# Kernel optimization log

Measured on AMD Instinct MI355X. Metric: run time of the kernel, lower is better.

Reference implementation:

```python
import jax, jax.numpy as jnp
import numpy as np

N_NODES = 50000
N_EDGES = 800000
IN_CH = 8
CH = 128
EATTR = 6
N_BBOX = 2000
N_CLASSES = 32
N_BLOCKS = 3  # head + 2 residual blocks; n_blocks_out = 3
FUSION = CH * N_BLOCKS  # 384


def _kaiming(key, shape):
    fan_in = shape[0]
    return jax.random.normal(key, shape, dtype=jnp.float32) * np.sqrt(2.0 / fan_in)


def setup_inputs() -> dict:
    key = jax.random.key(0)
    ks = jax.random.split(key, 24)
    x = jax.random.normal(ks[0], (N_NODES, IN_CH), dtype=jnp.float32)
    e_attr = jax.random.normal(ks[1], (N_EDGES, EATTR), dtype=jnp.float32)
    edge = jax.random.randint(ks[2], (2, N_EDGES), 0, N_NODES, dtype=jnp.int32)
    bbox_idx = jnp.sort(jax.random.randint(ks[3], (N_NODES,), 0, N_BBOX, dtype=jnp.int32))
    d_head = 2 * IN_CH + EATTR   # 22
    d_blk = 2 * CH + EATTR       # 262
    inp = {
        "x": x, "e_attr": e_attr,
        "W_h": _kaiming(ks[4], (d_head, CH)), "b_h": jnp.zeros((CH,), jnp.float32),
        "Ws_h": _kaiming(ks[5], (d_head, CH)), "bs_h": jnp.zeros((CH,), jnp.float32),
        "Wb": jnp.stack([_kaiming(ks[6], (d_blk, CH)), _kaiming(ks[7], (d_blk, CH))]),
        "bb": jnp.zeros((2, CH), jnp.float32),
        "Wbs": jnp.stack([_kaiming(ks[8], (d_blk, CH)), _kaiming(ks[9], (d_blk, CH))]),
        "bbs": jnp.zeros((2, CH), jnp.float32),
        "W_f": _kaiming(ks[10], (FUSION, 1024)), "b_f": jnp.zeros((1024,), jnp.float32),
        "W_fs": _kaiming(ks[11], (FUSION, 1024)), "b_fs": jnp.zeros((1024,), jnp.float32),
        "W1": _kaiming(ks[12], ((FUSION + 1024) * 2, 512)), "b1": jnp.zeros((512,), jnp.float32),
        "W2": _kaiming(ks[13], (512, 256)), "b2": jnp.zeros((256,), jnp.float32),
        "W3": _kaiming(ks[14], (256, N_CLASSES)), "b3": jnp.zeros((N_CLASSES,), jnp.float32),
        "edge": edge, "bbox_idx": bbox_idx,
    }
    return inp


def _seg_max0(h, idx, n):
    m = jax.ops.segment_max(h, idx, num_segments=n)
    return jnp.where(jnp.isneginf(m), 0.0, m)  # empty segments -> 0 (torch_scatter semantics)


def _seg_mean(h, idx, n):
    s = jax.ops.segment_sum(h, idx, num_segments=n)
    c = jax.ops.segment_sum(jnp.ones((h.shape[0], 1), h.dtype), idx, num_segments=n)
    return s / jnp.maximum(c, 1.0)


def _graph_conv(x, x_node, src, dst, e_attr, W, b, Ws, bs, n):
    # edge message: MLP(concat(x_i, x_j - x_i, e_attr)); max-scatter for node stream,
    # mean-scatter for super stream (gp2 = two global-pool reductions)
    h = jax.nn.relu(jnp.concatenate([x[src], x[dst] - x[src], e_attr], axis=1) @ W + b)
    f = _seg_max0(h, dst, n)
    hs = jax.nn.relu(jnp.concatenate([x_node[src], x_node[dst] - x_node[src], e_attr], axis=1) @ Ws + bs)
    f_super = _seg_mean(hs, dst, n)
    return f, f_super


def reference(x, e_attr, W_h, b_h, Ws_h, bs_h, Wb, bb, Wbs, bbs,
              W_f, b_f, W_fs, b_fs, W1, b1, W2, b2, W3, b3, edge, bbox_idx):
    src, dst = edge[0], edge[1]
    n = x.shape[0]
    # head conv
    f, fs = _graph_conv(x, x, src, dst, e_attr, W_h, b_h, Ws_h, bs_h, n)
    feats, feats_super = [f], [fs]
    # residual blocks
    for i in range(N_BLOCKS - 1):
        g, gs = _graph_conv(feats[-1], feats_super[-1], src, dst, e_attr,
                            Wb[i], bb[i], Wbs[i], bbs[i], n)
        feats.append(g + feats[-1])
        feats_super.append(gs + feats_super[-1])
    feats = jnp.concatenate(feats, axis=1)              # [N, 384]
    fusion = jax.nn.relu(feats @ W_f + b_f)             # [N, 1024]
    out_feat = jnp.concatenate([fusion, feats], axis=1) # [N, 1408]
    feats_super = jnp.concatenate(feats_super, axis=1)  # [N, 384]
    feats_super = _seg_mean(feats_super, bbox_idx, N_BBOX)            # [B, 384]
    fusion_super = jax.nn.relu(feats_super @ W_fs + b_fs)             # [B, 1024]
    out_super = jnp.concatenate([fusion_super, feats_super], axis=1)  # [B, 1408]
    pooled = _seg_max0(out_feat, bbox_idx, N_BBOX)                    # [B, 1408]
    h = jnp.concatenate([pooled, out_super], axis=1)                  # [B, 2816]
    h = jax.nn.relu(h @ W1 + b1)
    h = jax.nn.relu(h @ W2 + b2)  # dropout=0 / eval mode
    logits = h @ W3 + b3          # classifier == 'softmax': raw logits returned
    return logits
```

## Files before the change

### kernel.cpp

```cpp
#include <hip/hip_runtime.h>
#include <stdint.h>

#define NN      50000
#define NN_PAD  50176
#define NE      800000
#define INCH    8
#define CH      128
#define EA      6
#define NB      2000
#define NB_PAD  2048
#define NCLS    32
#define FUS     384
#define K1      2816
#define SCAN_NBLK 49

typedef _Float16 half8 __attribute__((ext_vector_type(8)));
typedef _Float16 h2 __attribute__((ext_vector_type(2)));
typedef float f32x4 __attribute__((ext_vector_type(4)));

__global__ __launch_bounds__(256) void k_deg(const int* __restrict__ edge,
                                             int* __restrict__ deg) {
  int e = blockIdx.x * 256 + threadIdx.x;
  if (e < NE) atomicAdd(&deg[edge[NE + e]], 1);
}

__global__ __launch_bounds__(1024) void k_scan1(const int* __restrict__ deg,
                                                int* __restrict__ row_ptr,
                                                int* __restrict__ bsum) {
  __shared__ int wsum[16];
  const int t = threadIdx.x, lane = t & 63, w = t >> 6;
  const int i = blockIdx.x * 1024 + t;
  int x = (i < NN) ? deg[i] : 0;
#pragma unroll
  for (int off = 1; off < 64; off <<= 1) {
    int y = __shfl_up(x, off, 64);
    if (lane >= off) x += y;
  }
  if (lane == 63) wsum[w] = x;
  __syncthreads();
  if (w == 0 && lane < 16) {
    int s = wsum[lane];
#pragma unroll
    for (int off = 1; off < 16; off <<= 1) {
      int y = __shfl_up(s, off, 64);
      if (lane >= off) s += y;
    }
    wsum[lane] = s;
  }
  __syncthreads();
  int incl = x + ((w == 0) ? 0 : wsum[w - 1]);
  if (i < NN) row_ptr[i + 1] = incl;
  if (t == 1023) bsum[blockIdx.x] = incl;
}

__global__ __launch_bounds__(64) void k_scan2(int* __restrict__ bsum) {
  const int t = threadIdx.x;
  int x = (t < SCAN_NBLK) ? bsum[t] : 0;
#pragma unroll
  for (int off = 1; off < 64; off <<= 1) {
    int y = __shfl_up(x, off, 64);
    if (t >= off) x += y;
  }
  int ex = __shfl_up(x, 1, 64);
  if (t == 0) ex = 0;
  if (t < SCAN_NBLK) bsum[t] = ex;
}

__global__ __launch_bounds__(256) void k_scan3(const int* __restrict__ bsum,
                                               int* __restrict__ row_ptr) {
  const int i = blockIdx.x * 256 + threadIdx.x;
  if (i == 0) row_ptr[0] = 0;
  if (i < NN) row_ptr[i + 1] += bsum[i >> 10];
}

__global__ __launch_bounds__(256) void k_fill(
    const int* __restrict__ edge, const float* __restrict__ eattr,
    const int* __restrict__ row_ptr, int* __restrict__ cursor,
    int* __restrict__ ssrc, _Float16* __restrict__ sea8) {
  int e = blockIdx.x * 256 + threadIdx.x;
  if (e >= NE) return;
  int s = edge[e], d = edge[NE + e];
  int idx = row_ptr[d] + atomicAdd(&cursor[d], 1);
  ssrc[idx] = s;
  half8 v;
#pragma unroll
  for (int j = 0; j < EA; ++j) v[j] = (_Float16)eattr[(size_t)e * EA + j];
  v[6] = (_Float16)0.f; v[7] = (_Float16)0.f;
  *(half8*)(sea8 + (size_t)idx * 8) = v;
}

__global__ __launch_bounds__(256) void k_segstart(const int* __restrict__ bbox,
                                                  int* __restrict__ seg) {
  int i = blockIdx.x * 256 + threadIdx.x;
  if (i >= NN) return;
  int bc = bbox[i];
  int bp = (i == 0) ? -1 : bbox[i - 1];
  for (int j = bp + 1; j <= bc; ++j) seg[j] = i;
  if (i == NN - 1)
    for (int j = bc + 1; j <= NB; ++j) seg[j] = NN;
}

__global__ __launch_bounds__(256) void k_node_pq(
    const float* __restrict__ X, int ldx, int K,
    const float* __restrict__ WN, const float* __restrict__ bN,
    const float* __restrict__ WS, const float* __restrict__ bS,
    _Float16* __restrict__ PQi, _Float16* __restrict__ Qi) {
  const int sel = blockIdx.y;
  const float* W = sel ? WS : WN;
  const float* bias = sel ? bS : bN;
  const int t = threadIdx.x, lane = t & 63, wv = t >> 6;
  const int nbase = blockIdx.x * 32 + wv * 8;
  const int c = lane * 2;
  const float2 bv = *(const float2*)(bias + c);
  float2 pacc[8], qacc[8];
#pragma unroll
  for (int u = 0; u < 8; ++u) { pacc[u] = bv; qacc[u] = make_float2(0.f, 0.f); }
  const int xrow = min(nbase + (lane >> 3), NN - 1);
  const int xk = lane & 7;
  for (int k0 = 0; k0 < K; k0 += 8) {
    const float xv = X[(size_t)xrow * ldx + k0 + xk];
#pragma unroll
    for (int j = 0; j < 8; ++j) {
      const float2 w1 = *(const float2*)(W + (size_t)(k0 + j) * CH + c);
      const float2 w2 = *(const float2*)(W + (size_t)(K + k0 + j) * CH + c);
      const float2 wd = {w1.x - w2.x, w1.y - w2.y};
#pragma unroll
      for (int u = 0; u < 8; ++u) {
        const float xs = __shfl(xv, u * 8 + j, 64);
        pacc[u].x += xs * wd.x; pacc[u].y += xs * wd.y;
        qacc[u].x += xs * w2.x; qacc[u].y += xs * w2.y;
      }
    }
  }
#pragma unroll
  for (int u = 0; u < 8; ++u) {
    const int node = nbase + u;
    if (node < NN) {
      const size_t o = ((size_t)node * 64 + lane) * 4 + sel * 2;
      *(h2*)(PQi + o) = (h2){(_Float16)pacc[u].x, (_Float16)pacc[u].y};
      *(h2*)(Qi + o)  = (h2){(_Float16)qacc[u].x, (_Float16)qacc[u].y};
    }
  }
}

__global__ __launch_bounds__(64) void k_cvtWnpq(
    const float* __restrict__ WbAll, const float* __restrict__ WbsAll,
    _Float16* __restrict__ whN, _Float16* __restrict__ whS) {
  const int blk = blockIdx.z;
  const float* W = (blockIdx.y ? WbsAll : WbAll) + (size_t)blk * 262 * CH;
  _Float16* wh   = (blockIdx.y ? whS : whN) + (size_t)blk * 32768;
  const int c = blockIdx.x >> 4, tile = blockIdx.x & 15;
  const int L = threadIdx.x;
  const int n = tile * 16 + (L & 15);
  const int k0 = c * 32 + (L >> 4) * 8;
  half8 v;
#pragma unroll
  for (int j = 0; j < 8; ++j) {
    const int k = k0 + j;
    float val;
    if (n < CH) val = W[(size_t)k * CH + n] - W[(size_t)(CH + k) * CH + n];
    else        val = W[(size_t)(CH + k) * CH + (n - CH)];
    v[j] = (_Float16)val;
  }
  *(half8*)(wh + (((size_t)(c * 16 + tile)) * 64 + L) * 8) = v;
}

__global__ __launch_bounds__(256) void k_npq_mfma(
    const _Float16* __restrict__ Xn, const _Float16* __restrict__ Xs, int ldx,
    const _Float16* __restrict__ whN, const _Float16* __restrict__ whS,
    const float* __restrict__ biasN, const float* __restrict__ biasS,
    _Float16* __restrict__ PQi, _Float16* __restrict__ Qi) {
  const int sel = blockIdx.y;
  const _Float16* X = sel ? Xs : Xn;
  const _Float16* wh = sel ? whS : whN;
  const float* bias = sel ? biasS : biasN;
  const int t = threadIdx.x, lane = t & 63, wv = t >> 6;
  const int nbase = blockIdx.x * 64;
  const int m = lane & 15, quad = lane >> 4;
  f32x4 acc[4][4];
#pragma unroll
  for (int i = 0; i < 4; ++i)
#pragma unroll
    for (int nt = 0; nt < 4; ++nt) acc[i][nt] = (f32x4){0.f, 0.f, 0.f, 0.f};
#pragma unroll
  for (int ks = 0; ks < 4; ++ks) {
    half8 b[4];
#pragma unroll
    for (int nt = 0; nt < 4; ++nt)
      b[nt] = *(const half8*)(wh + (((size_t)(ks * 16 + wv * 4 + nt)) * 64 + lane) * 8);
#pragma unroll
    for (int i = 0; i < 4; ++i) {
      const int row = min(nbase + i * 16 + m, NN - 1);
      const half8 a = *(const half8*)(X + (size_t)row * ldx + ks * 32 + quad * 8);
#pragma unroll
      for (int nt = 0; nt < 4; ++nt)
        acc[i][nt] = __builtin_amdgcn_mfma_f32_16x16x32_f16(a, b[nt], acc[i][nt],
                                                            0, 0, 0);
    }
  }
#pragma unroll
  for (int i = 0; i < 4; ++i)
#pragma unroll
    for (int nt = 0; nt < 4; ++nt) {
      const int col = wv * 64 + nt * 16 + m;
      const float bv = (col < CH) ? bias[col] : 0.f;
#pragma unroll
      for (int r = 0; r < 4; ++r) {
        const int row = nbase + i * 16 + quad * 4 + r;
        if (row < NN) {
          const float v = acc[i][nt][r] + bv;
          if (col < CH)
            PQi[((size_t)row * 64 + (col >> 1)) * 4 + sel * 2 + (col & 1)] =
                (_Float16)v;
          else {
            const int qc = col - CH;
            Qi[((size_t)row * 64 + (qc >> 1)) * 4 + sel * 2 + (qc & 1)] =
                (_Float16)v;
          }
        }
      }
    }
}

__global__ __launch_bounds__(256) void k_conv2(
    const int* __restrict__ row_ptr, const int* __restrict__ ssrc,
    const _Float16* __restrict__ sea8,
    const _Float16* __restrict__ PQi, const _Float16* __restrict__ Qi,
    const float* __restrict__ Cn, const float* __restrict__ Cs,
    _Float16* __restrict__ feats, _Float16* __restrict__ sfeats,
    int cur, int prev) {
  const int t = threadIdx.x;
  const int lane = t & 63;
  const int node = blockIdx.x * 4 + (t >> 6);
  const int c = lane * 2;
  h2 cwnh[EA], cwsh[EA];
#pragma unroll
  for (int j = 0; j < EA; ++j) {
    const float2 a = *(const float2*)(Cn + j * CH + c);
    const float2 b = *(const float2*)(Cs + j * CH + c);
    cwnh[j] = (h2){(_Float16)a.x, (_Float16)a.y};
    cwsh[j] = (h2){(_Float16)b.x, (_Float16)b.y};
  }
  int i0 = __builtin_amdgcn_readfirstlane(row_ptr[node]);
  int i1 = __builtin_amdgcn_readfirstlane(row_ptr[node + 1]);
  const uint2 qv = *(const uint2*)(Qi + ((size_t)node * 64 + lane) * 4);
  const h2 qnh = *(const h2*)&qv.x;
  const h2 qsh = *(const h2*)&qv.y;
  const _Float16* pqL = PQi + (size_t)lane * 4;
  h2 anh = (h2){(_Float16)0.f, (_Float16)0.f};
  float as0 = 0.f, as1 = 0.f;
  const h2 zero = (h2){(_Float16)0.f, (_Float16)0.f};
#define COMP(PV, J)                                                        \
  {                                                                        \
    unsigned w0 = __shfl((int)ea_l.x, (J), 64);                            \
    unsigned w1 = __shfl((int)ea_l.y, (J), 64);                            \
    unsigned w2 = __shfl((int)ea_l.z, (J), 64);                            \
    const h2 ea01 = *(const h2*)&w0;                                       \
    const h2 ea23 = *(const h2*)&w1;                                       \
    const h2 ea45 = *(const h2*)&w2;                                       \
    h2 vn = *(const h2*)&PV.x + qnh;                                       \
    h2 vs = *(const h2*)&PV.y + qsh;                                       \
    h2 b;                                                                  \
    b = (h2){ea01[0], ea01[0]}; vn += b * cwnh[0]; vs += b * cwsh[0];      \
    b = (h2){ea01[1], ea01[1]}; vn += b * cwnh[1]; vs += b * cwsh[1];      \
    b = (h2){ea23[0], ea23[0]}; vn += b * cwnh[2]; vs += b * cwsh[2];      \
    b = (h2){ea23[1], ea23[1]}; vn += b * cwnh[3]; vs += b * cwsh[3];      \
    b = (h2){ea45[0], ea45[0]}; vn += b * cwnh[4]; vs += b * cwsh[4];      \
    b = (h2){ea45[1], ea45[1]}; vn += b * cwnh[5]; vs += b * cwsh[5];      \
    anh = __builtin_elementwise_max(anh, vn);                              \
    const h2 vsr = __builtin_elementwise_max(vs, zero);                    \
    as0 += (float)vsr[0]; as1 += (float)vsr[1];                            \
  }
  for (int base = i0; base < i1; base += 64) {
    const int cnt = min(64, i1 - base);
    int s_l = 0;
    uint4 ea_l = {0u, 0u, 0u, 0u};
    if (lane < cnt) {
      s_l = ssrc[base + lane];
      ea_l = *(const uint4*)(sea8 + (size_t)(base + lane) * 8);
    }
    int j = 0;
    for (; j + 8 <= cnt; j += 8) {
      const int s0 = __shfl(s_l, j, 64),     s1 = __shfl(s_l, j + 1, 64);
      const int s2 = __shfl(s_l, j + 2, 64), s3 = __shfl(s_l, j + 3, 64);
      const int s4 = __shfl(s_l, j + 4, 64), s5 = __shfl(s_l, j + 5, 64);
      const int s6 = __shfl(s_l, j + 6, 64), s7 = __shfl(s_l, j + 7, 64);
      const uint2 p0 = *(const uint2*)(pqL + (size_t)s0 * 256);
      const uint2 p1 = *(const uint2*)(pqL + (size_t)s1 * 256);
      const uint2 p2 = *(const uint2*)(pqL + (size_t)s2 * 256);
      const uint2 p3 = *(const uint2*)(pqL + (size_t)s3 * 256);
      const uint2 p4 = *(const uint2*)(pqL + (size_t)s4 * 256);
      const uint2 p5 = *(const uint2*)(pqL + (size_t)s5 * 256);
      const uint2 p6 = *(const uint2*)(pqL + (size_t)s6 * 256);
      const uint2 p7 = *(const uint2*)(pqL + (size_t)s7 * 256);
      COMP(p0, j)     COMP(p1, j + 1) COMP(p2, j + 2) COMP(p3, j + 3)
      COMP(p4, j + 4) COMP(p5, j + 5) COMP(p6, j + 6) COMP(p7, j + 7)
    }
    for (; j + 4 <= cnt; j += 4) {
      const int s0 = __shfl(s_l, j, 64),     s1 = __shfl(s_l, j + 1, 64);
      const int s2 = __shfl(s_l, j + 2, 64), s3 = __shfl(s_l, j + 3, 64);
      const uint2 p0 = *(const uint2*)(pqL + (size_t)s0 * 256);
      const uint2 p1 = *(const uint2*)(pqL + (size_t)s1 * 256);
      const uint2 p2 = *(const uint2*)(pqL + (size_t)s2 * 256);
      const uint2 p3 = *(const uint2*)(pqL + (size_t)s3 * 256);
      COMP(p0, j) COMP(p1, j + 1) COMP(p2, j + 2) COMP(p3, j + 3)
    }
    for (; j < cnt; ++j) {
      const int s0 = __shfl(s_l, j, 64);
      const uint2 p0 = *(const uint2*)(pqL + (size_t)s0 * 256);
      COMP(p0, j)
    }
  }
#undef COMP
  float an0 = (float)anh[0], an1 = (float)anh[1];
  const float inv = 1.f / fmaxf((float)(i1 - i0), 1.f);
  as0 *= inv; as1 *= inv;
  const size_t o = (size_t)node * FUS + (size_t)cur * CH + c;
  if (prev >= 0) {
    const size_t op = (size_t)node * FUS + (size_t)prev * CH + c;
    const h2 prn = *(const h2*)(feats + op);
    const h2 prs = *(const h2*)(sfeats + op);
    an0 += (float)prn[0]; an1 += (float)prn[1];
    as0 += (float)prs[0]; as1 += (float)prs[1];
  }
  *(h2*)(feats + o)  = (h2){(_Float16)an0, (_Float16)an1};
  *(h2*)(sfeats + o) = (h2){(_Float16)as0, (_Float16)as1};
}

template <int N, int NT>
__global__ __launch_bounds__(64) void k_cvtB(const float* __restrict__ W,
                                             _Float16* __restrict__ wh) {
  const int c = blockIdx.x / NT;
  const int tile = blockIdx.x % NT;
  const int L = threadIdx.x;
  const int n = tile * 16 + (L & 15);
  const int k0 = c * 32 + (L >> 4) * 8;
  half8 v;
#pragma unroll
  for (int j = 0; j < 8; ++j) v[j] = (_Float16)W[(size_t)(k0 + j) * N + n];
  *(half8*)(wh + (((size_t)(c * NT + tile)) * 64 + L) * 8) = v;
}

template <int N, int NT>
__global__ __launch_bounds__(64) void k_cvtB2(const float* __restrict__ WA,
                                              const float* __restrict__ WB,
                                              _Float16* __restrict__ whA,
                                              _Float16* __restrict__ whB) {
  const float* W = blockIdx.y ? WB : WA;
  _Float16* wh   = blockIdx.y ? whB : whA;
  const int c = blockIdx.x / NT;
  const int tile = blockIdx.x % NT;
  const int L = threadIdx.x;
  const int n = tile * 16 + (L & 15);
  const int k0 = c * 32 + (L >> 4) * 8;
  half8 v;
#pragma unroll
  for (int j = 0; j < 8; ++j) v[j] = (_Float16)W[(size_t)(k0 + j) * N + n];
  *(half8*)(wh + (((size_t)(c * NT + tile)) * 64 + L) * 8) = v;
}

__global__ __launch_bounds__(256, 6) void k_pool_mfma(
    const _Float16* __restrict__ feats16, const _Float16* __restrict__ wh,
    const int* __restrict__ bbox, const float* __restrict__ bf,
    float* __restrict__ pooled) {
  __shared__ float cl[32 * 132];
  __shared__ int s_bb[64];
  _Float16* abuf = (_Float16*)cl;
  const int t = threadIdx.x, lane = t & 63, wv = t >> 6;
  const int fid = blockIdx.x;
  const int xcd = fid & 7, slot = fid >> 3;
  const int cg = slot & 7;
  const int rb = xcd * 98 + (slot >> 3);
  const int nbase = rb * 64;
  const int m = lane & 15, quad = lane >> 4;
  if (t < 64) s_bb[t] = bbox[min(nbase + t, NN - 1)];
  f32x4 acc[4][2];
#pragma unroll
  for (int i = 0; i < 4; ++i)
#pragma unroll
    for (int nt = 0; nt < 2; ++nt) acc[i][nt] = (f32x4){0.f, 0.f, 0.f, 0.f};
  const _Float16* apc = feats16 + (size_t)(nbase + wv * 16 + m) * FUS + quad * 8;
  const _Float16* bp = wh + ((size_t)(cg * 8 + wv * 2) * 64 + lane) * 8;
  _Float16* wslot = abuf + wv * 512 + lane * 8;
  const _Float16* rbase = abuf + lane * 8;
  half8 b0 = *(const half8*)(bp);
  half8 b1 = *(const half8*)(bp + 512);
  half8 rA = *(const half8*)(apc);
  *(half8*)(wslot) = rA;
  half8 rN = *(const half8*)(apc + 32);
  __syncthreads();
#pragma unroll
  for (int ks = 0; ks < 12; ++ks) {
    const int cur = ks & 1;
    half8 nb0, nb1;
    if (ks < 11) {
      nb0 = *(const half8*)(bp + (size_t)(ks + 1) * 32768);
      nb1 = *(const half8*)(bp + (size_t)(ks + 1) * 32768 + 512);
    }
#pragma unroll
    for (int i = 0; i < 4; ++i) {
      const half8 a = *(const half8*)(rbase + cur * 2048 + i * 512);
      acc[i][0] = __builtin_amdgcn_mfma_f32_16x16x32_f16(a, b0, acc[i][0], 0, 0, 0);
      acc[i][1] = __builtin_amdgcn_mfma_f32_16x16x32_f16(a, b1, acc[i][1], 0, 0, 0);
    }
    if (ks < 11) {
      *(half8*)(wslot + (cur ^ 1) * 2048) = rN;
      b0 = nb0; b1 = nb1;
    }
    if (ks < 10) rN = *(const half8*)(apc + (size_t)(ks + 2) * 32);
    __syncthreads();
  }
  const int col = t & 127, rh = t >> 7;
  const int gcol = cg * 128 + col;
  const float bias = bf[gcol];
  int curb = -1;
  float mx = 0.f;
#pragma unroll
  for (int p = 0; p < 2; ++p) {
    __syncthreads();
#pragma unroll
    for (int ii = 0; ii < 2; ++ii)
#pragma unroll
      for (int nt = 0; nt < 2; ++nt) {
        const int scol = wv * 32 + nt * 16 + m;
#pragma unroll
        for (int r = 0; r < 4; ++r)
          cl[(ii * 16 + quad * 4 + r) * 132 + scol] = acc[p + 2 * ii][nt][r];
      }
    __syncthreads();
    for (int rr = 0; rr < 16; ++rr) {
      const int g = rh * 32 + p * 16 + rr;
      const int node = nbase + g;
      if (node >= NN) break;
      const int bid = s_bb[g];
      const float v = fmaxf(cl[(rh * 16 + rr) * 132 + col] + bias, 0.f);
      if (bid != curb) {
        if (curb >= 0)
          atomicMax((unsigned*)(pooled + (size_t)curb * 1408 + gcol),
                    __float_as_uint(mx));
        curb = bid;
        mx = v;
      } else {
        mx = fmaxf(mx, v);
      }
    }
  }
  if (curb >= 0)
    atomicMax((unsigned*)(pooled + (size_t)curb * 1408 + gcol),
              __float_as_uint(mx));
}

__global__ __launch_bounds__(256) void k_poolraw(
    const _Float16* __restrict__ feats, const _Float16* __restrict__ sfeats,
    const int* __restrict__ seg, float* __restrict__ pooled,
    float* __restrict__ sb, _Float16* __restrict__ sbH) {
  const int b = blockIdx.x, t = threadIdx.x;
  if (t >= 192) return;
  const int c2 = t * 2;
  const int n0 = __builtin_amdgcn_readfirstlane(seg[b]);
  const int n1 = __builtin_amdgcn_readfirstlane(seg[b + 1]);
  float2 fmx = {0.f, 0.f}, ss = {0.f, 0.f};
  for (int n = n0; n < n1; ++n) {
    const h2 f2 = *(const h2*)(feats + (size_t)n * FUS + c2);
    fmx.x = fmaxf(fmx.x, (float)f2[0]); fmx.y = fmaxf(fmx.y, (float)f2[1]);
    const h2 s2 = *(const h2*)(sfeats + (size_t)n * FUS + c2);
    ss.x += (float)s2[0]; ss.y += (float)s2[1];
  }
  *(float2*)(pooled + (size_t)b * 1408 + 1024 + c2) = fmx;
  const float inv = 1.f / fmaxf((float)(n1 - n0), 1.f);
  float2 o = {ss.x * inv, ss.y * inv};
  *(float2*)(sb + (size_t)b * FUS + c2) = o;
  *(h2*)(sbH + (size_t)b * FUS + c2) = (h2){(_Float16)o.x, (_Float16)o.y};
}

__global__ __launch_bounds__(256) void k_fsup_mfma(
    const _Float16* __restrict__ sbH, const _Float16* __restrict__ wh,
    const float* __restrict__ bfs, float* __restrict__ fs) {
  const int t = threadIdx.x, lane = t & 63, wv = t >> 6;
  const int nbase = blockIdx.x * 64;
  const int cg = blockIdx.y;
  const int m = lane & 15, quad = lane >> 4;
  f32x4 acc[4][2];
#pragma unroll
  for (int i = 0; i < 4; ++i)
#pragma unroll
    for (int nt = 0; nt < 2; ++nt) acc[i][nt] = (f32x4){0.f, 0.f, 0.f, 0.f};
  const _Float16* ap = sbH + (size_t)(nbase + m) * FUS + quad * 8;
  const _Float16* bp = wh + ((size_t)(cg * 8 + wv * 2) * 64 + lane) * 8;
#pragma unroll
  for (int ks = 0; ks < 12; ++ks) {
    const half8 b0 = *(const half8*)(bp + (size_t)ks * 32768);
    const half8 b1v = *(const half8*)(bp + (size_t)ks * 32768 + 512);
#pragma unroll
    for (int i = 0; i < 4; ++i) {
      const half8 a = *(const half8*)(ap + (size_t)(i * 16) * FUS + ks * 32);
      acc[i][0] = __builtin_amdgcn_mfma_f32_16x16x32_f16(a, b0, acc[i][0], 0, 0, 0);
      acc[i][1] = __builtin_amdgcn_mfma_f32_16x16x32_f16(a, b1v, acc[i][1], 0, 0, 0);
    }
  }
#pragma unroll
  for (int i = 0; i < 4; ++i)
#pragma unroll
    for (int nt = 0; nt < 2; ++nt) {
      const int gcol = cg * 128 + wv * 32 + nt * 16 + m;
      const float bias = bfs[gcol];
#pragma unroll
      for (int r = 0; r < 4; ++r) {
        const int row = nbase + i * 16 + quad * 4 + r;
        if (row < NB)
          fs[(size_t)row * 1024 + gcol] = fmaxf(acc[i][nt][r] + bias, 0.f);
      }
    }
}

__global__ __launch_bounds__(256) void k_cvt_cat(
    const float* __restrict__ pooled, const float* __restrict__ fsup,
    const float* __restrict__ sb, _Float16* __restrict__ bbH) {
  const size_t off = ((size_t)blockIdx.x * 256 + threadIdx.x) * 8;
  const int row = (int)(off / K1);
  const int col = (int)(off - (size_t)row * K1);
  half8 v;
  if (row < NB) {
    const float* src;
    if (col < 1408)      src = pooled + (size_t)row * 1408 + col;
    else if (col < 2432) src = fsup + (size_t)row * 1024 + (col - 1408);
    else                 src = sb + (size_t)row * FUS + (col - 2432);
    const float4 f0 = *(const float4*)src;
    const float4 f1 = *(const float4*)(src + 4);
    v[0] = (_Float16)f0.x; v[1] = (_Float16)f0.y;
    v[2] = (_Float16)f0.z; v[3] = (_Float16)f0.w;
    v[4] = (_Float16)f1.x; v[5] = (_Float16)f1.y;
    v[6] = (_Float16)f1.z; v[7] = (_Float16)f1.w;
  } else {
#pragma unroll
    for (int j = 0; j < 8; ++j) v[j] = (_Float16)0.f;
  }
  *(half8*)(bbH + off) = v;
}

__global__ __launch_bounds__(256) void k_mlp1_mfma(
    const _Float16* __restrict__ bbH, const _Float16* __restrict__ wh,
    const float* __restrict__ b1, float* __restrict__ h1) {
  const int t = threadIdx.x, lane = t & 63, wv = t >> 6;
  const int nbase = blockIdx.x * 64;
  const int cg = blockIdx.y;
  const int m = lane & 15, quad = lane >> 4;
  f32x4 acc[4][2];
#pragma unroll
  for (int i = 0; i < 4; ++i)
#pragma unroll
    for (int nt = 0; nt < 2; ++nt) acc[i][nt] = (f32x4){0.f, 0.f, 0.f, 0.f};
  const _Float16* ap = bbH + (size_t)(nbase + m) * K1 + quad * 8;
  const _Float16* bp = wh + ((size_t)(cg * 8 + wv * 2) * 64 + lane) * 8;
#pragma unroll 4
  for (int ks = 0; ks < 88; ++ks) {
    const half8 b0 = *(const half8*)(bp + (size_t)ks * 16384);
    const half8 b1v = *(const half8*)(bp + (size_t)ks * 16384 + 512);
#pragma unroll
    for (int i = 0; i < 4; ++i) {
      const half8 a = *(const half8*)(ap + (size_t)(i * 16) * K1 + ks * 32);
      acc[i][0] = __builtin_amdgcn_mfma_f32_16x16x32_f16(a, b0, acc[i][0], 0, 0, 0);
      acc[i][1] = __builtin_amdgcn_mfma_f32_16x16x32_f16(a, b1v, acc[i][1], 0, 0, 0);
    }
  }
#pragma unroll
  for (int i = 0; i < 4; ++i)
#pragma unroll
    for (int nt = 0; nt < 2; ++nt) {
      const int gcol = cg * 128 + wv * 32 + nt * 16 + m;
      const float bias = b1[gcol];
#pragma unroll
      for (int r = 0; r < 4; ++r) {
        const int row = nbase + i * 16 + quad * 4 + r;
        if (row < NB)
          h1[(size_t)row * 512 + gcol] = fmaxf(acc[i][nt][r] + bias, 0.f);
      }
    }
}

__global__ __launch_bounds__(256) void k_mlp2(
    const float* __restrict__ h1, const float* __restrict__ W2,
    const float* __restrict__ b2, float* __restrict__ h2o) {
  const int r0 = blockIdx.x * 8, t = threadIdx.x;
  float acc[8];
#pragma unroll
  for (int u = 0; u < 8; ++u) acc[u] = 0.f;
  for (int k = 0; k < 512; ++k) {
    float w = W2[(size_t)k * 256 + t];
#pragma unroll
    for (int u = 0; u < 8; ++u) acc[u] += h1[(size_t)(r0 + u) * 512 + k] * w;
  }
  float bv = b2[t];
#pragma unroll
  for (int u = 0; u < 8; ++u)
    h2o[(size_t)(r0 + u) * 256 + t] = fmaxf(acc[u] + bv, 0.f);
}

__global__ __launch_bounds__(256) void k_mlp3(
    const float* __restrict__ h2i, const float* __restrict__ W3,
    const float* __restrict__ b3, float* __restrict__ out) {
  const int r0 = blockIdx.x * 8, t = threadIdx.x;
  const int u = t >> 5, oc = t & 31;
  const float* x = h2i + (size_t)(r0 + u) * 256;
  float acc = 0.f;
  for (int k = 0; k < 256; ++k) acc += x[k] * W3[(size_t)k * 32 + oc];
  out[(size_t)(r0 + u) * 32 + oc] = acc + b3[oc];
}

extern "C" void kernel_launch(void* const* d_in, const int* in_sizes, int n_in,
                              void* d_out, int out_size, void* d_ws, size_t ws_size,
                              hipStream_t stream) {
  const float* x     = (const float*)d_in[0];
  const float* eattr = (const float*)d_in[1];
  const float* W_h   = (const float*)d_in[2];
  const float* b_h   = (const float*)d_in[3];
  const float* Ws_h  = (const float*)d_in[4];
  const float* bs_h  = (const float*)d_in[5];
  const float* Wb    = (const float*)d_in[6];
  const float* bb    = (const float*)d_in[7];
  const float* Wbs   = (const float*)d_in[8];
  const float* bbs   = (const float*)d_in[9];
  const float* W_f   = (const float*)d_in[10];
  const float* b_f   = (const float*)d_in[11];
  const float* W_fs  = (const float*)d_in[12];
  const float* b_fs  = (const float*)d_in[13];
  const float* W1    = (const float*)d_in[14];
  const float* b1    = (const float*)d_in[15];
  const float* W2    = (const float*)d_in[16];
  const float* b2    = (const float*)d_in[17];
  const float* W3    = (const float*)d_in[18];
  const float* b3    = (const float*)d_in[19];
  const int*   edge  = (const int*)d_in[20];
  const int*   bbox  = (const int*)d_in[21];
  float* out = (float*)d_out;

  _Float16* feats  = (_Float16*)d_ws;
  _Float16* sfeats = feats + (size_t)NN_PAD * FUS;
  float* PQ = (float*)(sfeats + (size_t)NN_PAD * FUS);
  _Float16* PQi = (_Float16*)PQ;
  _Float16* Qi  = PQi + (size_t)NN * 256;
  float* sb   = PQ;
  float* fsup = sb + (size_t)NB * FUS;
  float* h1   = fsup + (size_t)NB * 1024;
  float* h2b  = h1 + (size_t)NB * 512;
  _Float16* bbH = (_Float16*)(h2b + (size_t)NB * 256);
  _Float16* W1H = bbH + (size_t)NB_PAD * K1;
  _Float16* WfH = (_Float16*)PQ + (size_t)784 * 12 * 2048;
  float* pooled = (float*)(WfH + (size_t)FUS * 1024);
  _Float16* sea8 = (_Float16*)(PQ + (size_t)2 * NN * CH);
  int* ssrc    = (int*)(sea8 + (size_t)NE * 8);
  int* row_ptr = ssrc + NE;
  int* deg     = row_ptr + NN + 1;
  int* cursor  = deg + NN;
  int* seg     = cursor + NN;
  _Float16* WcatN = (_Float16*)(seg + NB + 1);
  _Float16* WcatS = WcatN + (size_t)2 * 128 * 256;
  int* bsum = (int*)(WcatS + (size_t)2 * 128 * 256);
  _Float16* sbH = (_Float16*)(((uintptr_t)(bsum + SCAN_NBLK) + 127) &
                              ~(uintptr_t)127);
  _Float16* WfsH = sbH + (size_t)NB_PAD * FUS;

  hipMemsetAsync(deg, 0, 2 * NN * sizeof(int), stream);
  hipMemsetAsync(feats + (size_t)NN * FUS, 0,
                 (size_t)(NN_PAD - NN) * FUS * sizeof(_Float16), stream);

  k_deg<<<(NE + 255) / 256, 256, 0, stream>>>(edge, deg);
  k_scan1<<<SCAN_NBLK, 1024, 0, stream>>>(deg, row_ptr, bsum);
  k_scan2<<<1, 64, 0, stream>>>(bsum);
  k_scan3<<<(NN + 255) / 256, 256, 0, stream>>>(bsum, row_ptr);
  k_fill<<<(NE + 255) / 256, 256, 0, stream>>>(edge, eattr, row_ptr, cursor,
                                               ssrc, sea8);
  k_segstart<<<(NN + 255) / 256, 256, 0, stream>>>(bbox, seg);

  const int npq_grid = (NN + 31) / 32;

  k_node_pq<<<dim3(npq_grid, 2), 256, 0, stream>>>(x, INCH, INCH, W_h, b_h,
                                                   Ws_h, bs_h, PQi, Qi);
  k_conv2<<<NN / 4, 256, 0, stream>>>(row_ptr, ssrc, sea8, PQi, Qi,
                                      W_h + 2 * INCH * CH, Ws_h + 2 * INCH * CH,
                                      feats, sfeats, 0, -1);

  k_cvtWnpq<<<dim3(64, 2, 2), 64, 0, stream>>>(Wb, Wbs, WcatN, WcatS);
  for (int i = 0; i < 2; ++i) {
    const float* Wi  = Wb  + (size_t)i * 262 * CH;
    const float* bi  = bb  + (size_t)i * CH;
    const float* Wsi = Wbs + (size_t)i * 262 * CH;
    const float* bsi = bbs + (size_t)i * CH;
    k_npq_mfma<<<dim3((NN + 63) / 64, 2), 256, 0, stream>>>(
        feats + i * CH, sfeats + i * CH, FUS, WcatN + (size_t)i * 32768,
        WcatS + (size_t)i * 32768, bi, bsi, PQi, Qi);
    k_conv2<<<NN / 4, 256, 0, stream>>>(row_ptr, ssrc, sea8, PQi, Qi,
                                        Wi + 2 * CH * CH, Wsi + 2 * CH * CH,
                                        feats, sfeats, i + 1, i);
  }

  k_cvtB2<1024, 64><<<dim3(12 * 64, 2), 64, 0, stream>>>(W_f, W_fs, WfH, WfsH);
  hipMemsetAsync(pooled, 0, (size_t)NB * 1408 * sizeof(float), stream);
  k_pool_mfma<<<784 * 8, 256, 0, stream>>>(feats, WfH, bbox, b_f, pooled);
  k_poolraw<<<NB, 256, 0, stream>>>(feats, sfeats, seg, pooled, sb, sbH);
  k_fsup_mfma<<<dim3(NB_PAD / 64, 8), 256, 0, stream>>>(sbH, WfsH, b_fs, fsup);

  k_cvt_cat<<<(int)(((size_t)NB_PAD * K1 / 8) / 256), 256, 0, stream>>>(
      pooled, fsup, sb, bbH);
  k_cvtB<512, 32><<<88 * 32, 64, 0, stream>>>(W1, W1H);
  k_mlp1_mfma<<<dim3(NB_PAD / 64, 4), 256, 0, stream>>>(bbH, W1H, b1, h1);
  k_mlp2<<<NB / 8, 256, 0, stream>>>(h1, W2, b2, h2b);
  k_mlp3<<<NB / 8, 256, 0, stream>>>(h2b, W3, b3, out);
}
```

Measured before the change: 785.8 us.

## Load pool GEMM A operands directly from global, retile waves 2x2

The pooling fusion GEMM kernel stops staging A rows through shared memory with double-buffering and per-k-step barriers. Each wave now covers a 32-row by 64-column sub-tile and loads A and B fragments straight from global memory each k-step. This removes twelve __syncthreads and the LDS traffic, at the cost of redundant global A loads across waves, no software prefetch, and more registers.

```diff
diff --git a/kernel.cpp b/kernel.cpp
--- a/kernel.cpp
+++ b/kernel.cpp
@@ -365,7 +365,6 @@
     float* __restrict__ pooled) {
   __shared__ float cl[32 * 132];
   __shared__ int s_bb[64];
-  _Float16* abuf = (_Float16*)cl;
   const int t = threadIdx.x, lane = t & 63, wv = t >> 6;
   const int fid = blockIdx.x;
   const int xcd = fid & 7, slot = fid >> 3;
@@ -374,41 +373,29 @@
   const int nbase = rb * 64;
   const int m = lane & 15, quad = lane >> 4;
   if (t < 64) s_bb[t] = bbox[min(nbase + t, NN - 1)];
-  f32x4 acc[4][2];
-#pragma unroll
-  for (int i = 0; i < 4; ++i)
-#pragma unroll
-    for (int nt = 0; nt < 2; ++nt) acc[i][nt] = (f32x4){0.f, 0.f, 0.f, 0.f};
-  const _Float16* apc = feats16 + (size_t)(nbase + wv * 16 + m) * FUS + quad * 8;
-  const _Float16* bp = wh + ((size_t)(cg * 8 + wv * 2) * 64 + lane) * 8;
-  _Float16* wslot = abuf + wv * 512 + lane * 8;
-  const _Float16* rbase = abuf + lane * 8;
-  half8 b0 = *(const half8*)(bp);
-  half8 b1 = *(const half8*)(bp + 512);
-  half8 rA = *(const half8*)(apc);
-  *(half8*)(wslot) = rA;
-  half8 rN = *(const half8*)(apc + 32);
-  __syncthreads();
+  const int rg = wv >> 1, ch = wv & 1;
+  f32x4 acc[2][4];
+#pragma unroll
+  for (int i = 0; i < 2; ++i)
+#pragma unroll
+    for (int nt = 0; nt < 4; ++nt) acc[i][nt] = (f32x4){0.f, 0.f, 0.f, 0.f};
+  const _Float16* ap = feats16 + (size_t)(nbase + rg * 32 + m) * FUS + quad * 8;
+  const _Float16* bp = wh + ((size_t)(cg * 8 + ch * 4) * 64 + lane) * 8;
 #pragma unroll
   for (int ks = 0; ks < 12; ++ks) {
-    const int cur = ks & 1;
-    half8 nb0, nb1;
-    if (ks < 11) {
-      nb0 = *(const half8*)(bp + (size_t)(ks + 1) * 32768);
-      nb1 = *(const half8*)(bp + (size_t)(ks + 1) * 32768 + 512);
-    }
-#pragma unroll
-    for (int i = 0; i < 4; ++i) {
-      const half8 a = *(const half8*)(rbase + cur * 2048 + i * 512);
-      acc[i][0] = __builtin_amdgcn_mfma_f32_16x16x32_f16(a, b0, acc[i][0], 0, 0, 0);
-      acc[i][1] = __builtin_amdgcn_mfma_f32_16x16x32_f16(a, b1, acc[i][1], 0, 0, 0);
-    }
-    if (ks < 11) {
-      *(half8*)(wslot + (cur ^ 1) * 2048) = rN;
-      b0 = nb0; b1 = nb1;
-    }
-    if (ks < 10) rN = *(const half8*)(apc + (size_t)(ks + 2) * 32);
-    __syncthreads();
+    half8 b[4], a[2];
+#pragma unroll
+    for (int nt = 0; nt < 4; ++nt)
+      b[nt] = *(const half8*)(bp + (size_t)ks * 32768 + nt * 512);
+#pragma unroll
+    for (int i = 0; i < 2; ++i)
+      a[i] = *(const half8*)(ap + (size_t)(i * 16) * FUS + ks * 32);
+#pragma unroll
+    for (int i = 0; i < 2; ++i)
+#pragma unroll
+      for (int nt = 0; nt < 4; ++nt)
+        acc[i][nt] = __builtin_amdgcn_mfma_f32_16x16x32_f16(a[i], b[nt],
+                                                            acc[i][nt], 0, 0, 0);
   }
   const int col = t & 127, rh = t >> 7;
   const int gcol = cg * 128 + col;
@@ -419,14 +406,12 @@
   for (int p = 0; p < 2; ++p) {
     __syncthreads();
 #pragma unroll
-    for (int ii = 0; ii < 2; ++ii)
-#pragma unroll
-      for (int nt = 0; nt < 2; ++nt) {
-        const int scol = wv * 32 + nt * 16 + m;
-#pragma unroll
-        for (int r = 0; r < 4; ++r)
-          cl[(ii * 16 + quad * 4 + r) * 132 + scol] = acc[p + 2 * ii][nt][r];
-      }
+    for (int nt = 0; nt < 4; ++nt) {
+      const int scol = ch * 64 + nt * 16 + m;
+#pragma unroll
+      for (int r = 0; r < 4; ++r)
+        cl[(rg * 16 + quad * 4 + r) * 132 + scol] = acc[p][nt][r];
+    }
     __syncthreads();
     for (int rr = 0; rr < 16; ++rr) {
       const int g = rh * 32 + p * 16 + rr;
```

Measured after the change: 818.1 us. +4.1%, slower.
